# Kernel tuning notes

Hardware: AMD Instinct MI355X
Metric: run time of the kernel (lower is better)

Reference implementation:

```python
import jax, jax.numpy as jnp
import numpy as np


def setup_inputs() -> dict:
    key = jax.random.key(0)
    k1, k2 = jax.random.split(key)
    B, L, H = 32, 512, 768   # batch, seq_len, hidden
    E, M, S = 32, 8, 4       # entities, mentions/entity, span tokens/mention
    token_reprs = jax.random.normal(k1, (B, L, H), dtype=jnp.float32)
    pos_idx = jax.random.randint(k2, (B, E, M, S), 0, L, dtype=jnp.int64)
    return {"token_reprs": token_reprs, "pos_idx": pos_idx}


def reference(token_reprs, pos_idx):
    # token_reprs: [B, L, H]; pos_idx: [B, E, M, S] token indices
    # gather span tokens per mention: [B, E, M, S, H]
    gathered = jax.vmap(lambda t, p: t[p])(token_reprs, pos_idx)
    # mean over span tokens -> mention reprs [B, E, M, H]
    mentions_reprs = jnp.mean(gathered, axis=3)
    # mean over mentions -> entity reprs [B, E, H]
    entity_reprs = jnp.mean(mentions_reprs, axis=2)
    # mention mask (all mentions valid in the dense regularization): [B, E, M]
    mentions_mask = jnp.ones(mentions_reprs.shape[:3], dtype=mentions_reprs.dtype)
    return (entity_reprs, mentions_reprs, mentions_mask)
```

## Files before the change

### kernel.cpp

```cpp
#include <hip/hip_runtime.h>
#include <hip/hip_bf16.h>


#define B_  32
#define L_  512
#define H_  768
#define E_  32
#define M_  8
#define S_  4
#define H4_ (H_ / 4)

#define ENT_ELEMS   (B_ * E_ * H_)
#define MEN_ELEMS   (B_ * E_ * M_ * H_)
#define MEN_OFFSET  ENT_ELEMS
#define MASK_OFFSET (ENT_ELEMS + MEN_ELEMS)

__global__ __launch_bounds__(H4_) void entity_repr_kernel(
    const float* __restrict__ tok,
    const int*   __restrict__ idx,
    float*       __restrict__ out)
{
    const int be = blockIdx.x;
    const int b  = be >> 5;
    const int t  = threadIdx.x;

    const float4* tb = (const float4*)(tok) + (size_t)b * L_ * H4_;
    const int*    ip = idx + (size_t)be * (M_ * S_);

    float4* ent_out = (float4*)(out) + (size_t)be * H4_;
    float4* men_out = (float4*)(out + MEN_OFFSET) + (size_t)be * (M_ * H4_);

    float ex = 0.f, ey = 0.f, ez = 0.f, ew = 0.f;

    #pragma unroll
    for (int m = 0; m < M_; ++m) {
        const int i0 = ip[m * S_ + 0];
        const int i1 = ip[m * S_ + 1];
        const int i2 = ip[m * S_ + 2];
        const int i3 = ip[m * S_ + 3];

        const float4 a = tb[(size_t)i0 * H4_ + t];
        const float4 c = tb[(size_t)i1 * H4_ + t];
        const float4 d = tb[(size_t)i2 * H4_ + t];
        const float4 e = tb[(size_t)i3 * H4_ + t];

        float4 mn;
        mn.x = (a.x + c.x + d.x + e.x) * 0.25f;
        mn.y = (a.y + c.y + d.y + e.y) * 0.25f;
        mn.z = (a.z + c.z + d.z + e.z) * 0.25f;
        mn.w = (a.w + c.w + d.w + e.w) * 0.25f;

        men_out[(size_t)m * H4_ + t] = mn;

        ex += mn.x; ey += mn.y; ez += mn.z; ew += mn.w;
    }

    float4 ev;
    ev.x = ex * (1.0f / M_);
    ev.y = ey * (1.0f / M_);
    ev.z = ez * (1.0f / M_);
    ev.w = ew * (1.0f / M_);
    ent_out[t] = ev;

    if (t < M_) {
        out[MASK_OFFSET + (size_t)be * M_ + t] = 1.0f;
    }
}

extern "C" void kernel_launch(void* const* d_in, const int* in_sizes, int n_in,
                              void* d_out, int out_size, void* d_ws, size_t ws_size,
                              hipStream_t stream) {
    const float* tok = (const float*)d_in[0];
    const int*   idx = (const int*)d_in[1];
    float*       out = (float*)d_out;

    dim3 grid(B_ * E_);
    dim3 block(H4_);
    entity_repr_kernel<<<grid, block, 0, stream>>>(tok, idx, out);
}
```

Baseline: 96.88 us.

## Split fused kernel into per-mention gather kernel and entity reduction kernel

Replaces the single per-entity kernel with two launches. The first uses one block per mention to gather and average span tokens. The second re-reads the stored mention representations to average them into entity representations. This raises the number of blocks eightfold to expose more memory-level parallelism for the random gathers. The cost is an extra kernel launch and re-reading the mention output from memory.

```diff
diff --git a/kernel.cpp b/kernel.cpp
--- a/kernel.cpp
+++ b/kernel.cpp
@@ -15,43 +15,50 @@
 #define MEN_OFFSET  ENT_ELEMS
 #define MASK_OFFSET (ENT_ELEMS + MEN_ELEMS)
 
-__global__ __launch_bounds__(H4_) void entity_repr_kernel(
+__global__ __launch_bounds__(H4_) void mention_kernel(
     const float* __restrict__ tok,
     const int*   __restrict__ idx,
     float*       __restrict__ out)
 {
+    const int bem = blockIdx.x;
+    const int be  = bem >> 3;
+    const int b   = be >> 5;
+    const int t   = threadIdx.x;
+
+    const float4* tb = (const float4*)(tok) + (size_t)b * L_ * H4_;
+    const int*    ip = idx + (size_t)bem * S_;
+
+    const int i0 = ip[0];
+    const int i1 = ip[1];
+    const int i2 = ip[2];
+    const int i3 = ip[3];
+
+    const float4 a = tb[(size_t)i0 * H4_ + t];
+    const float4 c = tb[(size_t)i1 * H4_ + t];
+    const float4 d = tb[(size_t)i2 * H4_ + t];
+    const float4 e = tb[(size_t)i3 * H4_ + t];
+
+    float4 mn;
+    mn.x = (a.x + c.x + d.x + e.x) * 0.25f;
+    mn.y = (a.y + c.y + d.y + e.y) * 0.25f;
+    mn.z = (a.z + c.z + d.z + e.z) * 0.25f;
+    mn.w = (a.w + c.w + d.w + e.w) * 0.25f;
+
+    ((float4*)(out + MEN_OFFSET))[(size_t)bem * H4_ + t] = mn;
+}
+
+__global__ __launch_bounds__(H4_) void entity_kernel(
+    float* __restrict__ out)
+{
     const int be = blockIdx.x;
-    const int b  = be >> 5;
     const int t  = threadIdx.x;
 
-    const float4* tb = (const float4*)(tok) + (size_t)b * L_ * H4_;
-    const int*    ip = idx + (size_t)be * (M_ * S_);
-
-    float4* ent_out = (float4*)(out) + (size_t)be * H4_;
-    float4* men_out = (float4*)(out + MEN_OFFSET) + (size_t)be * (M_ * H4_);
+    const float4* men = (const float4*)(out + MEN_OFFSET) + (size_t)be * (M_ * H4_);
 
     float ex = 0.f, ey = 0.f, ez = 0.f, ew = 0.f;
-
     #pragma unroll
     for (int m = 0; m < M_; ++m) {
-        const int i0 = ip[m * S_ + 0];
-        const int i1 = ip[m * S_ + 1];
-        const int i2 = ip[m * S_ + 2];
-        const int i3 = ip[m * S_ + 3];
-
-        const float4 a = tb[(size_t)i0 * H4_ + t];
-        const float4 c = tb[(size_t)i1 * H4_ + t];
-        const float4 d = tb[(size_t)i2 * H4_ + t];
-        const float4 e = tb[(size_t)i3 * H4_ + t];
-
-        float4 mn;
-        mn.x = (a.x + c.x + d.x + e.x) * 0.25f;
-        mn.y = (a.y + c.y + d.y + e.y) * 0.25f;
-        mn.z = (a.z + c.z + d.z + e.z) * 0.25f;
-        mn.w = (a.w + c.w + d.w + e.w) * 0.25f;
-
-        men_out[(size_t)m * H4_ + t] = mn;
-
+        const float4 mn = men[(size_t)m * H4_ + t];
         ex += mn.x; ey += mn.y; ez += mn.z; ew += mn.w;
     }
 
@@ -60,7 +67,7 @@
     ev.y = ey * (1.0f / M_);
     ev.z = ez * (1.0f / M_);
     ev.w = ew * (1.0f / M_);
-    ent_out[t] = ev;
+    ((float4*)(out))[(size_t)be * H4_ + t] = ev;
 
     if (t < M_) {
         out[MASK_OFFSET + (size_t)be * M_ + t] = 1.0f;
@@ -74,7 +81,6 @@
     const int*   idx = (const int*)d_in[1];
     float*       out = (float*)d_out;
 
-    dim3 grid(B_ * E_);
-    dim3 block(H4_);
-    entity_repr_kernel<<<grid, block, 0, stream>>>(tok, idx, out);
+    mention_kernel<<<dim3(B_ * E_ * M_), dim3(H4_), 0, stream>>>(tok, idx, out);
+    entity_kernel <<<dim3(B_ * E_),      dim3(H4_), 0, stream>>>(out);
 }
```

New measurement: 99.33 us. 1.03x slower.

## Split mentions across 768-thread blocks with XCD-aware remap and nontemporal stores

Applied to the files above, without the earlier changes.

Each block now uses 768 threads: four groups each handle two mentions, and the entity mean is reduced through shared memory. Block IDs are remapped so that all entities of one batch land on the same XCD, which should improve L2 reuse of the gathered token rows. Output stores use nontemporal hints to avoid polluting the cache. The trade-off is a syncthreads and an LDS reduction per block, plus larger blocks that may lower occupancy flexibility.

```diff
diff --git a/kernel.cpp b/kernel.cpp
--- a/kernel.cpp
+++ b/kernel.cpp
@@ -15,55 +15,63 @@
 #define MEN_OFFSET  ENT_ELEMS
 #define MASK_OFFSET (ENT_ELEMS + MEN_ELEMS)
 
-__global__ __launch_bounds__(H4_) void entity_repr_kernel(
+typedef float v4f __attribute__((ext_vector_type(4)));
+
+__global__ __launch_bounds__(768) void entity_repr_fused(
     const float* __restrict__ tok,
     const int*   __restrict__ idx,
     float*       __restrict__ out)
 {
-    const int be = blockIdx.x;
-    const int b  = be >> 5;
-    const int t  = threadIdx.x;
+    const int s   = blockIdx.x;
+    const int xcd = s & 7;
+    const int j   = s >> 3;
+    const int b   = xcd + 8 * (j >> 5);
+    const int e   = j & 31;
+    const int be  = b * E_ + e;
 
-    const float4* tb = (const float4*)(tok) + (size_t)b * L_ * H4_;
-    const int*    ip = idx + (size_t)be * (M_ * S_);
+    const int t    = threadIdx.x;
+    const int mgrp = t / 192;
+    const int col  = t - mgrp * 192;
 
-    float4* ent_out = (float4*)(out) + (size_t)be * H4_;
-    float4* men_out = (float4*)(out + MEN_OFFSET) + (size_t)be * (M_ * H4_);
+    const v4f* tb = (const v4f*)(tok) + (size_t)b * L_ * H4_;
+    const int* ip = idx + (size_t)be * (M_ * S_);
 
-    float ex = 0.f, ey = 0.f, ez = 0.f, ew = 0.f;
+    v4f* men_out = (v4f*)(out + MEN_OFFSET) + (size_t)be * (M_ * H4_);
+
+    v4f acc = (v4f)(0.f);
 
     #pragma unroll
-    for (int m = 0; m < M_; ++m) {
+    for (int mm = 0; mm < 2; ++mm) {
+        const int m  = mgrp + mm * 4;
         const int i0 = ip[m * S_ + 0];
         const int i1 = ip[m * S_ + 1];
         const int i2 = ip[m * S_ + 2];
         const int i3 = ip[m * S_ + 3];
 
-        const float4 a = tb[(size_t)i0 * H4_ + t];
-        const float4 c = tb[(size_t)i1 * H4_ + t];
-        const float4 d = tb[(size_t)i2 * H4_ + t];
-        const float4 e = tb[(size_t)i3 * H4_ + t];
+        const v4f g0 = tb[(size_t)i0 * H4_ + col];
+        const v4f g1 = tb[(size_t)i1 * H4_ + col];
+        const v4f g2 = tb[(size_t)i2 * H4_ + col];
+        const v4f g3 = tb[(size_t)i3 * H4_ + col];
 
-        float4 mn;
-        mn.x = (a.x + c.x + d.x + e.x) * 0.25f;
-        mn.y = (a.y + c.y + d.y + e.y) * 0.25f;
-        mn.z = (a.z + c.z + d.z + e.z) * 0.25f;
-        mn.w = (a.w + c.w + d.w + e.w) * 0.25f;
+        const v4f mn = (g0 + g1 + g2 + g3) * 0.25f;
 
-        men_out[(size_t)m * H4_ + t] = mn;
+        __builtin_nontemporal_store(mn, &men_out[(size_t)m * H4_ + col]);
 
-        ex += mn.x; ey += mn.y; ez += mn.z; ew += mn.w;
+        acc += mn;
     }
 
-    float4 ev;
-    ev.x = ex * (1.0f / M_);
-    ev.y = ey * (1.0f / M_);
-    ev.z = ez * (1.0f / M_);
-    ev.w = ew * (1.0f / M_);
-    ent_out[t] = ev;
+    __shared__ v4f red[4][H4_];
+    red[mgrp][col] = acc;
+    __syncthreads();
+
+    if (mgrp == 0) {
+        const v4f r = (red[0][col] + red[1][col] + red[2][col] + red[3][col])
+                      * (1.0f / M_);
+        __builtin_nontemporal_store(r, &((v4f*)out)[(size_t)be * H4_ + col]);
+    }
 
     if (t < M_) {
-        out[MASK_OFFSET + (size_t)be * M_ + t] = 1.0f;
+        __builtin_nontemporal_store(1.0f, &out[MASK_OFFSET + (size_t)be * M_ + t]);
     }
 }
 
@@ -74,7 +82,5 @@
     const int*   idx = (const int*)d_in[1];
     float*       out = (float*)d_out;
 
-    dim3 grid(B_ * E_);
-    dim3 block(H4_);
-    entity_repr_kernel<<<grid, block, 0, stream>>>(tok, idx, out);
+    entity_repr_fused<<<dim3(B_ * E_), dim3(768), 0, stream>>>(tok, idx, out);
 }
```

Result: faster. 94.10 us (-2.9%).
